# Optimization experiments

Measured on AMD Instinct MI355X. Metric: run time of the kernel, lower is better.

The kernel has to match this reference:

```python
import jax, jax.numpy as jnp
import numpy as np

B, N, C, H = 4096, 49, 128, 4
DH = C // H  # head dim = 32
SCALE = DH ** -0.5

def setup_inputs() -> dict:
    key = jax.random.key(0)
    kx, kq, kp, kb = jax.random.split(key, 4)
    x = jax.random.normal(kx, (B, N, C), dtype=jnp.float32)
    w_qkv = jax.random.normal(kq, (C, 3 * C), dtype=jnp.float32) * (C ** -0.5)
    w_proj = jax.random.normal(kp, (C, C), dtype=jnp.float32) * (C ** -0.5)
    b_proj = jax.random.normal(kb, (C,), dtype=jnp.float32) * 0.01
    return {"x": x, "w_qkv": w_qkv, "w_proj": w_proj, "b_proj": b_proj}

def reference(x, w_qkv, w_proj, b_proj):
    Bx, Nx, Cx = x.shape
    qkv = x @ w_qkv  # (B, N, 3C)
    q, k, v = jnp.split(qkv, 3, axis=-1)
    # (B, N, C) -> (B, H, N, DH)
    def heads(t):
        return t.reshape(Bx, Nx, H, DH).transpose(0, 2, 1, 3)
    q, k, v = heads(q), heads(k), heads(v)
    attn = jnp.einsum('bhnd,bhmd->bhnm', q, k) * SCALE
    attn = jax.nn.softmax(attn, axis=-1)
    out = jnp.einsum('bhnm,bhmd->bhnd', attn, v)
    out = out.transpose(0, 2, 1, 3).reshape(Bx, Nx, Cx)
    return out @ w_proj + b_proj
```

## Files before the change

### kernel.cpp

```cpp
#include <hip/hip_runtime.h>
#include <hip/hip_bf16.h>

typedef unsigned short u16;
typedef unsigned int u32;
typedef __bf16 bf16;
typedef __attribute__((ext_vector_type(8))) __bf16 bf16x8;
typedef __attribute__((ext_vector_type(4))) __bf16 bf16x4;
typedef __attribute__((ext_vector_type(4))) float f32x4;

#define MFMA16(A,B,C) __builtin_amdgcn_mfma_f32_16x16x32_bf16(A,B,C,0,0,0)

constexpr int NTOK = 49;
constexpr int CH   = 128;
constexpr float CEXP = 0.17677669529663687f * 1.4426950408889634f;

__device__ __forceinline__ bf16x8 lds_v8(const char* p) {
    return *reinterpret_cast<const bf16x8*>(p);
}
__device__ __forceinline__ void lds_st64(char* p, float a0, float a1, float a2, float a3) {
    bf16x4 v = {(bf16)a0, (bf16)a1, (bf16)a2, (bf16)a3};
    *reinterpret_cast<bf16x4*>(p) = v;
}
__device__ __forceinline__ u32 pkbf(float a, float b) {
    u16 lo = __builtin_bit_cast(u16, (bf16)a);
    u16 hi = __builtin_bit_cast(u16, (bf16)b);
    return (u32)lo | ((u32)hi << 16);
}

__device__ __forceinline__ bf16x8 xchg(u32 lo0, u32 lo1, u32 hi0, u32 hi1,
                                       int srcA, int srcB, bool hiT) {
    u32 a0 = __shfl(lo0, srcA), b0 = __shfl(hi0, srcA);
    u32 a1 = __shfl(lo1, srcA), b1 = __shfl(hi1, srcA);
    u32 a2 = __shfl(lo0, srcB), b2 = __shfl(hi0, srcB);
    u32 a3 = __shfl(lo1, srcB), b3 = __shfl(hi1, srcB);
    uint4 u = { hiT ? b0 : a0, hiT ? b1 : a1, hiT ? b2 : a2, hiT ? b3 : a3 };
    return __builtin_bit_cast(bf16x8, u);
}

__global__ void prep_weights_kernel(const float* __restrict__ wqkv,
                                    const float* __restrict__ wproj,
                                    bf16* __restrict__ ws) {
    int i = blockIdx.x * 256 + threadIdx.x;
    if (i < 384 * 128) {
        int n = i >> 7, k = i & 127;
        ws[i] = (bf16)wqkv[k * 384 + n];
    }
    if (i < 128 * 128) {
        int n = i >> 7, k = i & 127;
        ws[384 * 128 + i] = (bf16)wproj[k * 128 + n];
    }
}

__launch_bounds__(256, 4)
__global__ void fused_window_attn(const float* __restrict__ x,
                                  const bf16* __restrict__ wqkv_t,
                                  const bf16* __restrict__ wproj_t,
                                  const float* __restrict__ bias,
                                  float* __restrict__ out) {
    __shared__ __align__(16) u16 smem[16384];
    char* S8 = reinterpret_cast<char*>(smem);

    const int tid  = threadIdx.x;
    const int blk  = blockIdx.x;
    const int h    = tid >> 6;
    const int lane = tid & 63;
    const int lr   = lane & 15;
    const int lg   = lane >> 4;
    const int srcA = lr + 32 * (lg & 1);
    const int srcB = srcA + 16;
    const bool hiT = (lg >= 2);

    char* Vb = S8 + 16384 + h * 4096;

    const float* xw = x + (size_t)blk * (NTOK * CH);
    #pragma unroll
    for (int it = 0; it < 7; ++it) {
        int i = tid + it * 256;
        if (i < (NTOK * CH) / 4) {
            float4 v = reinterpret_cast<const float4*>(xw)[i];
            int e = i * 4, row = e >> 7, col = e & 127;
            bf16x4 pk4 = { (bf16)v.x, (bf16)v.y, (bf16)v.z, (bf16)v.w };
            *reinterpret_cast<bf16x4*>(S8 + row * 256 + ((col * 2) ^ ((row & 7) << 4))) = pk4;
        }
    }
    if (tid < 240) {
        uint4 zz = {0, 0, 0, 0};
        *reinterpret_cast<uint4*>(S8 + 49 * 256 + tid * 16) = zz;
    }

    bf16x8 wfv[2][4];
    #pragma unroll
    for (int half = 0; half < 2; ++half) {
        const bf16* wrow = wqkv_t + ((16 + 2 * h + half) * 16 + lr) * 128 + lg * 8;
        #pragma unroll
        for (int ks = 0; ks < 4; ++ks)
            wfv[half][ks] = *reinterpret_cast<const bf16x8*>(wrow + ks * 32);
    }
    __syncthreads();

    bf16x8 xf[4][4];
    #pragma unroll
    for (int tt = 0; tt < 4; ++tt)
        #pragma unroll
        for (int ks = 0; ks < 4; ++ks) {
            int row = tt * 16 + lr;
            xf[tt][ks] = lds_v8(S8 + row * 256 + ((ks * 64 + lg * 16) ^ ((row & 7) << 4)));
        }

    __builtin_amdgcn_s_setprio(1);
    #pragma unroll
    for (int i = 0; i < 2; ++i) {
        int dh = i * 16 + lr;
        #pragma unroll
        for (int tt = 0; tt < 4; ++tt) {
            f32x4 a = {0.f, 0.f, 0.f, 0.f};
            #pragma unroll
            for (int ks = 0; ks < 4; ++ks) a = MFMA16(xf[tt][ks], wfv[i][ks], a);
            lds_st64(Vb + dh * 128 + ((tt * 32 + lg * 8) ^ ((dh & 7) << 4)),
                     a[0], a[1], a[2], a[3]);
        }
    }

    bf16x8 qf[4];
    {
        u32 pkq[2][4][2];
        #pragma unroll
        for (int half = 0; half < 2; ++half) {
            int ct = 2 * h + half;
            bf16x8 wf[4];
            const bf16* wrow = wqkv_t + (ct * 16 + lr) * 128 + lg * 8;
            #pragma unroll
            for (int ks = 0; ks < 4; ++ks)
                wf[ks] = *reinterpret_cast<const bf16x8*>(wrow + ks * 32);
            #pragma unroll
            for (int tt = 0; tt < 4; ++tt) {
                f32x4 a = {0.f, 0.f, 0.f, 0.f};
                #pragma unroll
                for (int ks = 0; ks < 4; ++ks) a = MFMA16(wf[ks], xf[tt][ks], a);
                pkq[half][tt][0] = pkbf(a[0], a[1]);
                pkq[half][tt][1] = pkbf(a[2], a[3]);
            }
        }
        #pragma unroll
        for (int tt = 0; tt < 4; ++tt)
            qf[tt] = xchg(pkq[0][tt][0], pkq[0][tt][1],
                          pkq[1][tt][0], pkq[1][tt][1], srcA, srcB, hiT);
    }
    bf16x8 kf[4];
    {
        u32 pkk[2][4][2];
        #pragma unroll
        for (int half = 0; half < 2; ++half) {
            int ct = 8 + 2 * h + half;
            bf16x8 wf[4];
            const bf16* wrow = wqkv_t + (ct * 16 + lr) * 128 + lg * 8;
            #pragma unroll
            for (int ks = 0; ks < 4; ++ks)
                wf[ks] = *reinterpret_cast<const bf16x8*>(wrow + ks * 32);
            #pragma unroll
            for (int tt = 0; tt < 4; ++tt) {
                f32x4 a = {0.f, 0.f, 0.f, 0.f};
                #pragma unroll
                for (int ks = 0; ks < 4; ++ks) a = MFMA16(wf[ks], xf[tt][ks], a);
                pkk[half][tt][0] = pkbf(a[0], a[1]);
                pkk[half][tt][1] = pkbf(a[2], a[3]);
            }
        }
        #pragma unroll
        for (int tt = 0; tt < 4; ++tt)
            kf[tt] = xchg(pkk[0][tt][0], pkk[0][tt][1],
                          pkk[1][tt][0], pkk[1][tt][1], srcA, srcB, hiT);
    }
    __builtin_amdgcn_s_setprio(0);

    bf16x8 vf[2][2];
    #pragma unroll
    for (int dht = 0; dht < 2; ++dht)
        #pragma unroll
        for (int ks2 = 0; ks2 < 2; ++ks2) {
            int dh = dht * 16 + lr;
            vf[dht][ks2] = lds_v8(Vb + dh * 128 + ((ks2 * 64 + lg * 16) ^ ((dh & 7) << 4)));
        }
    __syncthreads();

    bf16x8 ones;
    #pragma unroll
    for (int j = 0; j < 8; ++j) ones[j] = (bf16)1.0f;

    #pragma unroll
    for (int qt = 0; qt < 4; ++qt) {
        f32x4 s[4];
        __builtin_amdgcn_s_setprio(1);
        #pragma unroll
        for (int st = 0; st < 4; ++st) {
            f32x4 z = {0.f, 0.f, 0.f, 0.f};
            s[st] = MFMA16(kf[st], qf[qt], z);
        }
        __builtin_amdgcn_s_setprio(0);
        #pragma unroll
        for (int st = 0; st < 3; ++st)
            #pragma unroll
            for (int rg = 0; rg < 4; ++rg)
                s[st][rg] = exp2f(s[st][rg] * CEXP);
        {
            float e48 = exp2f(s[3][0] * CEXP);
            s[3][0] = (lg == 0) ? e48 : 0.f;
            s[3][1] = 0.f; s[3][2] = 0.f; s[3][3] = 0.f;
        }

        u32 pks[4][2];
        #pragma unroll
        for (int st = 0; st < 4; ++st) {
            pks[st][0] = pkbf(s[st][0], s[st][1]);
            pks[st][1] = pkbf(s[st][2], s[st][3]);
        }
        bf16x8 pf0 = xchg(pks[0][0], pks[0][1], pks[1][0], pks[1][1], srcA, srcB, hiT);
        bf16x8 pf1 = xchg(pks[2][0], pks[2][1], pks[3][0], pks[3][1], srcA, srcB, hiT);

        __builtin_amdgcn_s_setprio(1);
        f32x4 lacc = {0.f, 0.f, 0.f, 0.f};
        lacc = MFMA16(ones, pf0, lacc);
        lacc = MFMA16(ones, pf1, lacc);

        f32x4 o0 = {0.f, 0.f, 0.f, 0.f}, o1 = {0.f, 0.f, 0.f, 0.f};
        o0 = MFMA16(vf[0][0], pf0, o0);
        o1 = MFMA16(vf[1][0], pf0, o1);
        o0 = MFMA16(vf[0][1], pf1, o0);
        o1 = MFMA16(vf[1][1], pf1, o1);
        __builtin_amdgcn_s_setprio(0);
        float rs = 1.f / lacc[0];

        int q = qt * 16 + lr;
        lds_st64(S8 + q * 256 + ((h * 64 + lg * 8) ^ ((q & 7) << 4)),
                 o0[0] * rs, o0[1] * rs, o0[2] * rs, o0[3] * rs);
        lds_st64(S8 + q * 256 + ((h * 64 + 32 + lg * 8) ^ ((q & 7) << 4)),
                 o1[0] * rs, o1[1] * rs, o1[2] * rs, o1[3] * rs);
    }
    __syncthreads();

    bf16x8 ofr[4][4];
    #pragma unroll
    for (int tt = 0; tt < 4; ++tt)
        #pragma unroll
        for (int ks = 0; ks < 4; ++ks) {
            int row = tt * 16 + lr;
            ofr[tt][ks] = lds_v8(S8 + row * 256 + ((ks * 64 + lg * 16) ^ ((row & 7) << 4)));
        }
    #pragma unroll
    for (int i = 0; i < 2; ++i) {
        int ct = 2 * h + i;
        bf16x8 wf[4];
        const bf16* wrow = wproj_t + (ct * 16 + lr) * 128 + lg * 8;
        #pragma unroll
        for (int ks = 0; ks < 4; ++ks)
            wf[ks] = *reinterpret_cast<const bf16x8*>(wrow + ks * 32);
        float4 bv = *reinterpret_cast<const float4*>(bias + ct * 16 + lg * 4);
        __builtin_amdgcn_s_setprio(1);
        #pragma unroll
        for (int tt = 0; tt < 4; ++tt) {
            f32x4 a = {0.f, 0.f, 0.f, 0.f};
            #pragma unroll
            for (int ks = 0; ks < 4; ++ks) a = MFMA16(wf[ks], ofr[tt][ks], a);
            int tok = tt * 16 + lr;
            if (tok < NTOK) {
                float4 r = { a[0] + bv.x, a[1] + bv.y, a[2] + bv.z, a[3] + bv.w };
                *reinterpret_cast<float4*>(
                    out + ((size_t)blk * NTOK + tok) * CH + ct * 16 + lg * 4) = r;
            }
        }
        __builtin_amdgcn_s_setprio(0);
    }
}

extern "C" void kernel_launch(void* const* d_in, const int* in_sizes, int n_in,
                              void* d_out, int out_size, void* d_ws, size_t ws_size,
                              hipStream_t stream) {
    const float* x     = (const float*)d_in[0];
    const float* wqkv  = (const float*)d_in[1];
    const float* wproj = (const float*)d_in[2];
    const float* bias  = (const float*)d_in[3];
    float* out = (float*)d_out;
    bf16* ws   = (bf16*)d_ws;

    constexpr size_t WS_NEED = (size_t)(384 * 128 + 128 * 128) * sizeof(u16);
    if (ws_size < WS_NEED) return;

    prep_weights_kernel<<<192, 256, 0, stream>>>(wqkv, wproj, ws);
    fused_window_attn<<<4096, 256, 0, stream>>>(x, ws, ws + 384 * 128, bias, out);
}
```

Before: 89.59 us.

## Process two windows per block and prefetch next window's input during attention

Each block now handles two consecutive windows, so half as many blocks are launched. While the first window's QKV projection finishes, the second window's input is loaded from global memory into registers, then written into the now-free LDS region after a barrier. The aim is to overlap global load latency with compute and to amortize the block launch and weight load cost. In exchange it adds register pressure (14 extra staging registers), extra barriers, and halves the grid, which may hurt occupancy and load balance.

```diff
diff --git a/kernel.cpp b/kernel.cpp
--- a/kernel.cpp
+++ b/kernel.cpp
@@ -59,6 +59,8 @@
                                   float* __restrict__ out) {
     __shared__ __align__(16) u16 smem[16384];
     char* S8 = reinterpret_cast<char*>(smem);
+    char* XR = S8;
+    char* VR = S8 + 16384;
 
     const int tid  = threadIdx.x;
     const int blk  = blockIdx.x;
@@ -70,24 +72,26 @@
     const int srcB = srcA + 16;
     const bool hiT = (lg >= 2);
 
-    char* Vb = S8 + 16384 + h * 4096;
-
-    const float* xw = x + (size_t)blk * (NTOK * CH);
-    #pragma unroll
-    for (int it = 0; it < 7; ++it) {
-        int i = tid + it * 256;
-        if (i < (NTOK * CH) / 4) {
-            float4 v = reinterpret_cast<const float4*>(xw)[i];
-            int e = i * 4, row = e >> 7, col = e & 127;
-            bf16x4 pk4 = { (bf16)v.x, (bf16)v.y, (bf16)v.z, (bf16)v.w };
-            *reinterpret_cast<bf16x4*>(S8 + row * 256 + ((col * 2) ^ ((row & 7) << 4))) = pk4;
+    char* Vb = VR + h * 4096;
+    const size_t wbase = (size_t)blk * 2;
+
+    {
+        const float* xw = x + wbase * (NTOK * CH);
+        #pragma unroll
+        for (int it = 0; it < 7; ++it) {
+            int i = tid + it * 256;
+            if (i < (NTOK * CH) / 4) {
+                float4 v = reinterpret_cast<const float4*>(xw)[i];
+                int e = i * 4, row = e >> 7, col = e & 127;
+                bf16x4 pk4 = { (bf16)v.x, (bf16)v.y, (bf16)v.z, (bf16)v.w };
+                *reinterpret_cast<bf16x4*>(XR + row * 256 + ((col * 2) ^ ((row & 7) << 4))) = pk4;
+            }
         }
     }
     if (tid < 240) {
         uint4 zz = {0, 0, 0, 0};
-        *reinterpret_cast<uint4*>(S8 + 49 * 256 + tid * 16) = zz;
-    }
-
+        *reinterpret_cast<uint4*>(XR + 49 * 256 + tid * 16) = zz;
+    }
     bf16x8 wfv[2][4];
     #pragma unroll
     for (int half = 0; half < 2; ++half) {
@@ -98,177 +102,215 @@
     }
     __syncthreads();
 
-    bf16x8 xf[4][4];
-    #pragma unroll
-    for (int tt = 0; tt < 4; ++tt)
-        #pragma unroll
-        for (int ks = 0; ks < 4; ++ks) {
-            int row = tt * 16 + lr;
-            xf[tt][ks] = lds_v8(S8 + row * 256 + ((ks * 64 + lg * 16) ^ ((row & 7) << 4)));
-        }
-
-    __builtin_amdgcn_s_setprio(1);
-    #pragma unroll
-    for (int i = 0; i < 2; ++i) {
-        int dh = i * 16 + lr;
-        #pragma unroll
-        for (int tt = 0; tt < 4; ++tt) {
-            f32x4 a = {0.f, 0.f, 0.f, 0.f};
-            #pragma unroll
-            for (int ks = 0; ks < 4; ++ks) a = MFMA16(xf[tt][ks], wfv[i][ks], a);
-            lds_st64(Vb + dh * 128 + ((tt * 32 + lg * 8) ^ ((dh & 7) << 4)),
-                     a[0], a[1], a[2], a[3]);
-        }
-    }
-
-    bf16x8 qf[4];
-    {
-        u32 pkq[2][4][2];
-        #pragma unroll
-        for (int half = 0; half < 2; ++half) {
-            int ct = 2 * h + half;
-            bf16x8 wf[4];
-            const bf16* wrow = wqkv_t + (ct * 16 + lr) * 128 + lg * 8;
-            #pragma unroll
-            for (int ks = 0; ks < 4; ++ks)
-                wf[ks] = *reinterpret_cast<const bf16x8*>(wrow + ks * 32);
-            #pragma unroll
-            for (int tt = 0; tt < 4; ++tt) {
-                f32x4 a = {0.f, 0.f, 0.f, 0.f};
-                #pragma unroll
-                for (int ks = 0; ks < 4; ++ks) a = MFMA16(wf[ks], xf[tt][ks], a);
-                pkq[half][tt][0] = pkbf(a[0], a[1]);
-                pkq[half][tt][1] = pkbf(a[2], a[3]);
-            }
-        }
-        #pragma unroll
-        for (int tt = 0; tt < 4; ++tt)
-            qf[tt] = xchg(pkq[0][tt][0], pkq[0][tt][1],
-                          pkq[1][tt][0], pkq[1][tt][1], srcA, srcB, hiT);
-    }
-    bf16x8 kf[4];
-    {
-        u32 pkk[2][4][2];
-        #pragma unroll
-        for (int half = 0; half < 2; ++half) {
-            int ct = 8 + 2 * h + half;
-            bf16x8 wf[4];
-            const bf16* wrow = wqkv_t + (ct * 16 + lr) * 128 + lg * 8;
-            #pragma unroll
-            for (int ks = 0; ks < 4; ++ks)
-                wf[ks] = *reinterpret_cast<const bf16x8*>(wrow + ks * 32);
-            #pragma unroll
-            for (int tt = 0; tt < 4; ++tt) {
-                f32x4 a = {0.f, 0.f, 0.f, 0.f};
-                #pragma unroll
-                for (int ks = 0; ks < 4; ++ks) a = MFMA16(wf[ks], xf[tt][ks], a);
-                pkk[half][tt][0] = pkbf(a[0], a[1]);
-                pkk[half][tt][1] = pkbf(a[2], a[3]);
-            }
-        }
-        #pragma unroll
-        for (int tt = 0; tt < 4; ++tt)
-            kf[tt] = xchg(pkk[0][tt][0], pkk[0][tt][1],
-                          pkk[1][tt][0], pkk[1][tt][1], srcA, srcB, hiT);
-    }
-    __builtin_amdgcn_s_setprio(0);
-
-    bf16x8 vf[2][2];
-    #pragma unroll
-    for (int dht = 0; dht < 2; ++dht)
-        #pragma unroll
-        for (int ks2 = 0; ks2 < 2; ++ks2) {
-            int dh = dht * 16 + lr;
-            vf[dht][ks2] = lds_v8(Vb + dh * 128 + ((ks2 * 64 + lg * 16) ^ ((dh & 7) << 4)));
-        }
-    __syncthreads();
-
     bf16x8 ones;
     #pragma unroll
     for (int j = 0; j < 8; ++j) ones[j] = (bf16)1.0f;
 
-    #pragma unroll
-    for (int qt = 0; qt < 4; ++qt) {
-        f32x4 s[4];
+    u32 xst[14];
+
+    #pragma unroll 1
+    for (int w = 0; w < 2; ++w) {
+        bf16x8 xf[4][4];
+        #pragma unroll
+        for (int tt = 0; tt < 4; ++tt)
+            #pragma unroll
+            for (int ks = 0; ks < 4; ++ks) {
+                int row = tt * 16 + lr;
+                xf[tt][ks] = lds_v8(XR + row * 256 + ((ks * 64 + lg * 16) ^ ((row & 7) << 4)));
+            }
+
         __builtin_amdgcn_s_setprio(1);
         #pragma unroll
-        for (int st = 0; st < 4; ++st) {
-            f32x4 z = {0.f, 0.f, 0.f, 0.f};
-            s[st] = MFMA16(kf[st], qf[qt], z);
+        for (int i = 0; i < 2; ++i) {
+            int dh = i * 16 + lr;
+            #pragma unroll
+            for (int tt = 0; tt < 4; ++tt) {
+                f32x4 a = {0.f, 0.f, 0.f, 0.f};
+                #pragma unroll
+                for (int ks = 0; ks < 4; ++ks) a = MFMA16(xf[tt][ks], wfv[i][ks], a);
+                lds_st64(Vb + dh * 128 + ((tt * 32 + lg * 8) ^ ((dh & 7) << 4)),
+                         a[0], a[1], a[2], a[3]);
+            }
+        }
+        bf16x8 qf[4];
+        {
+            u32 pkq[2][4][2];
+            #pragma unroll
+            for (int half = 0; half < 2; ++half) {
+                int ct = 2 * h + half;
+                bf16x8 wf[4];
+                const bf16* wrow = wqkv_t + (ct * 16 + lr) * 128 + lg * 8;
+                #pragma unroll
+                for (int ks = 0; ks < 4; ++ks)
+                    wf[ks] = *reinterpret_cast<const bf16x8*>(wrow + ks * 32);
+                #pragma unroll
+                for (int tt = 0; tt < 4; ++tt) {
+                    f32x4 a = {0.f, 0.f, 0.f, 0.f};
+                    #pragma unroll
+                    for (int ks = 0; ks < 4; ++ks) a = MFMA16(wf[ks], xf[tt][ks], a);
+                    pkq[half][tt][0] = pkbf(a[0], a[1]);
+                    pkq[half][tt][1] = pkbf(a[2], a[3]);
+                }
+            }
+            #pragma unroll
+            for (int tt = 0; tt < 4; ++tt)
+                qf[tt] = xchg(pkq[0][tt][0], pkq[0][tt][1],
+                              pkq[1][tt][0], pkq[1][tt][1], srcA, srcB, hiT);
+        }
+        bf16x8 kf[4];
+        {
+            u32 pkk[2][4][2];
+            #pragma unroll
+            for (int half = 0; half < 2; ++half) {
+                int ct = 8 + 2 * h + half;
+                bf16x8 wf[4];
+                const bf16* wrow = wqkv_t + (ct * 16 + lr) * 128 + lg * 8;
+                #pragma unroll
+                for (int ks = 0; ks < 4; ++ks)
+                    wf[ks] = *reinterpret_cast<const bf16x8*>(wrow + ks * 32);
+                #pragma unroll
+                for (int tt = 0; tt < 4; ++tt) {
+                    f32x4 a = {0.f, 0.f, 0.f, 0.f};
+                    #pragma unroll
+                    for (int ks = 0; ks < 4; ++ks) a = MFMA16(wf[ks], xf[tt][ks], a);
+                    pkk[half][tt][0] = pkbf(a[0], a[1]);
+                    pkk[half][tt][1] = pkbf(a[2], a[3]);
+                }
+            }
+            #pragma unroll
+            for (int tt = 0; tt < 4; ++tt)
+                kf[tt] = xchg(pkk[0][tt][0], pkk[0][tt][1],
+                              pkk[1][tt][0], pkk[1][tt][1], srcA, srcB, hiT);
         }
         __builtin_amdgcn_s_setprio(0);
-        #pragma unroll
-        for (int st = 0; st < 3; ++st)
-            #pragma unroll
-            for (int rg = 0; rg < 4; ++rg)
-                s[st][rg] = exp2f(s[st][rg] * CEXP);
-        {
-            float e48 = exp2f(s[3][0] * CEXP);
-            s[3][0] = (lg == 0) ? e48 : 0.f;
-            s[3][1] = 0.f; s[3][2] = 0.f; s[3][3] = 0.f;
-        }
-
-        u32 pks[4][2];
-        #pragma unroll
-        for (int st = 0; st < 4; ++st) {
-            pks[st][0] = pkbf(s[st][0], s[st][1]);
-            pks[st][1] = pkbf(s[st][2], s[st][3]);
-        }
-        bf16x8 pf0 = xchg(pks[0][0], pks[0][1], pks[1][0], pks[1][1], srcA, srcB, hiT);
-        bf16x8 pf1 = xchg(pks[2][0], pks[2][1], pks[3][0], pks[3][1], srcA, srcB, hiT);
-
-        __builtin_amdgcn_s_setprio(1);
-        f32x4 lacc = {0.f, 0.f, 0.f, 0.f};
-        lacc = MFMA16(ones, pf0, lacc);
-        lacc = MFMA16(ones, pf1, lacc);
-
-        f32x4 o0 = {0.f, 0.f, 0.f, 0.f}, o1 = {0.f, 0.f, 0.f, 0.f};
-        o0 = MFMA16(vf[0][0], pf0, o0);
-        o1 = MFMA16(vf[1][0], pf0, o1);
-        o0 = MFMA16(vf[0][1], pf1, o0);
-        o1 = MFMA16(vf[1][1], pf1, o1);
-        __builtin_amdgcn_s_setprio(0);
-        float rs = 1.f / lacc[0];
-
-        int q = qt * 16 + lr;
-        lds_st64(S8 + q * 256 + ((h * 64 + lg * 8) ^ ((q & 7) << 4)),
-                 o0[0] * rs, o0[1] * rs, o0[2] * rs, o0[3] * rs);
-        lds_st64(S8 + q * 256 + ((h * 64 + 32 + lg * 8) ^ ((q & 7) << 4)),
-                 o1[0] * rs, o1[1] * rs, o1[2] * rs, o1[3] * rs);
-    }
-    __syncthreads();
-
-    bf16x8 ofr[4][4];
-    #pragma unroll
-    for (int tt = 0; tt < 4; ++tt)
-        #pragma unroll
-        for (int ks = 0; ks < 4; ++ks) {
-            int row = tt * 16 + lr;
-            ofr[tt][ks] = lds_v8(S8 + row * 256 + ((ks * 64 + lg * 16) ^ ((row & 7) << 4)));
-        }
-    #pragma unroll
-    for (int i = 0; i < 2; ++i) {
-        int ct = 2 * h + i;
-        bf16x8 wf[4];
-        const bf16* wrow = wproj_t + (ct * 16 + lr) * 128 + lg * 8;
-        #pragma unroll
-        for (int ks = 0; ks < 4; ++ks)
-            wf[ks] = *reinterpret_cast<const bf16x8*>(wrow + ks * 32);
-        float4 bv = *reinterpret_cast<const float4*>(bias + ct * 16 + lg * 4);
-        __builtin_amdgcn_s_setprio(1);
-        #pragma unroll
-        for (int tt = 0; tt < 4; ++tt) {
-            f32x4 a = {0.f, 0.f, 0.f, 0.f};
-            #pragma unroll
-            for (int ks = 0; ks < 4; ++ks) a = MFMA16(wf[ks], ofr[tt][ks], a);
-            int tok = tt * 16 + lr;
-            if (tok < NTOK) {
-                float4 r = { a[0] + bv.x, a[1] + bv.y, a[2] + bv.z, a[3] + bv.w };
-                *reinterpret_cast<float4*>(
-                    out + ((size_t)blk * NTOK + tok) * CH + ct * 16 + lg * 4) = r;
-            }
-        }
-        __builtin_amdgcn_s_setprio(0);
+
+        if (w == 0) {
+            const float* xn = x + (wbase + 1) * (NTOK * CH);
+            #pragma unroll
+            for (int it = 0; it < 7; ++it) {
+                int i = tid + it * 256;
+                if (i < (NTOK * CH) / 4) {
+                    float4 v = reinterpret_cast<const float4*>(xn)[i];
+                    xst[2 * it]     = pkbf(v.x, v.y);
+                    xst[2 * it + 1] = pkbf(v.z, v.w);
+                }
+            }
+        }
+
+        bf16x8 vf[2][2];
+        #pragma unroll
+        for (int dht = 0; dht < 2; ++dht)
+            #pragma unroll
+            for (int ks2 = 0; ks2 < 2; ++ks2) {
+                int dh = dht * 16 + lr;
+                vf[dht][ks2] = lds_v8(Vb + dh * 128 + ((ks2 * 64 + lg * 16) ^ ((dh & 7) << 4)));
+            }
+        __syncthreads();
+
+        if (w == 0) {
+            #pragma unroll
+            for (int it = 0; it < 7; ++it) {
+                int i = tid + it * 256;
+                if (i < (NTOK * CH) / 4) {
+                    int e = i * 4, row = e >> 7, col = e & 127;
+                    uint2 uv = { xst[2 * it], xst[2 * it + 1] };
+                    *reinterpret_cast<uint2*>(XR + row * 256 + ((col * 2) ^ ((row & 7) << 4))) = uv;
+                }
+            }
+        }
+
+        #pragma unroll
+        for (int qt = 0; qt < 4; ++qt) {
+            f32x4 s[4];
+            __builtin_amdgcn_s_setprio(1);
+            #pragma unroll
+            for (int st = 0; st < 4; ++st) {
+                f32x4 z = {0.f, 0.f, 0.f, 0.f};
+                s[st] = MFMA16(kf[st], qf[qt], z);
+            }
+            __builtin_amdgcn_s_setprio(0);
+            #pragma unroll
+            for (int st = 0; st < 3; ++st)
+                #pragma unroll
+                for (int rg = 0; rg < 4; ++rg)
+                    s[st][rg] = exp2f(s[st][rg] * CEXP);
+            {
+                float e48 = exp2f(s[3][0] * CEXP);
+                s[3][0] = (lg == 0) ? e48 : 0.f;
+                s[3][1] = 0.f; s[3][2] = 0.f; s[3][3] = 0.f;
+            }
+            u32 pks[4][2];
+            #pragma unroll
+            for (int st = 0; st < 4; ++st) {
+                pks[st][0] = pkbf(s[st][0], s[st][1]);
+                pks[st][1] = pkbf(s[st][2], s[st][3]);
+            }
+            bf16x8 pf0 = xchg(pks[0][0], pks[0][1], pks[1][0], pks[1][1], srcA, srcB, hiT);
+            bf16x8 pf1 = xchg(pks[2][0], pks[2][1], pks[3][0], pks[3][1], srcA, srcB, hiT);
+
+            __builtin_amdgcn_s_setprio(1);
+            f32x4 lacc = {0.f, 0.f, 0.f, 0.f};
+            lacc = MFMA16(ones, pf0, lacc);
+            lacc = MFMA16(ones, pf1, lacc);
+            f32x4 o0 = {0.f, 0.f, 0.f, 0.f}, o1 = {0.f, 0.f, 0.f, 0.f};
+            o0 = MFMA16(vf[0][0], pf0, o0);
+            o1 = MFMA16(vf[1][0], pf0, o1);
+            o0 = MFMA16(vf[0][1], pf1, o0);
+            o1 = MFMA16(vf[1][1], pf1, o1);
+            __builtin_amdgcn_s_setprio(0);
+            float rs = 1.f / lacc[0];
+
+            int q = qt * 16 + lr;
+            lds_st64(VR + q * 256 + ((h * 64 + lg * 8) ^ ((q & 7) << 4)),
+                     o0[0] * rs, o0[1] * rs, o0[2] * rs, o0[3] * rs);
+            lds_st64(VR + q * 256 + ((h * 64 + 32 + lg * 8) ^ ((q & 7) << 4)),
+                     o1[0] * rs, o1[1] * rs, o1[2] * rs, o1[3] * rs);
+        }
+        if (w == 0) {
+            #pragma unroll
+            for (int half = 0; half < 2; ++half) {
+                const bf16* wrow = wqkv_t + ((16 + 2 * h + half) * 16 + lr) * 128 + lg * 8;
+                #pragma unroll
+                for (int ks = 0; ks < 4; ++ks)
+                    wfv[half][ks] = *reinterpret_cast<const bf16x8*>(wrow + ks * 32);
+            }
+        }
+        __syncthreads();
+
+        bf16x8 ofr[4][4];
+        #pragma unroll
+        for (int tt = 0; tt < 4; ++tt)
+            #pragma unroll
+            for (int ks = 0; ks < 4; ++ks) {
+                int row = tt * 16 + lr;
+                ofr[tt][ks] = lds_v8(VR + row * 256 + ((ks * 64 + lg * 16) ^ ((row & 7) << 4)));
+            }
+        if (w == 0) __syncthreads();
+
+        #pragma unroll
+        for (int i = 0; i < 2; ++i) {
+            int ct = 2 * h + i;
+            bf16x8 wf[4];
+            const bf16* wrow = wproj_t + (ct * 16 + lr) * 128 + lg * 8;
+            #pragma unroll
+            for (int ks = 0; ks < 4; ++ks)
+                wf[ks] = *reinterpret_cast<const bf16x8*>(wrow + ks * 32);
+            float4 bv = *reinterpret_cast<const float4*>(bias + ct * 16 + lg * 4);
+            __builtin_amdgcn_s_setprio(1);
+            #pragma unroll
+            for (int tt = 0; tt < 4; ++tt) {
+                f32x4 a = {0.f, 0.f, 0.f, 0.f};
+                #pragma unroll
+                for (int ks = 0; ks < 4; ++ks) a = MFMA16(wf[ks], ofr[tt][ks], a);
+                int tok = tt * 16 + lr;
+                if (tok < NTOK) {
+                    float4 r = { a[0] + bv.x, a[1] + bv.y, a[2] + bv.z, a[3] + bv.w };
+                    *reinterpret_cast<float4*>(
+                        out + ((wbase + w) * NTOK + tok) * CH + ct * 16 + lg * 4) = r;
+                }
+            }
+            __builtin_amdgcn_s_setprio(0);
+        }
     }
 }
 
@@ -286,5 +328,5 @@
     if (ws_size < WS_NEED) return;
 
     prep_weights_kernel<<<192, 256, 0, stream>>>(wqkv, wproj, ws);
-    fused_window_attn<<<4096, 256, 0, stream>>>(x, ws, ws + 384 * 128, bias, out);
-}
+    fused_window_attn<<<2048, 256, 0, stream>>>(x, ws, ws + 384 * 128, bias, out);
+}
```

After: 310.8 us. 3.47x slower.
